# Kernel optimization log

Measured on AMD Instinct MI355X. Metric: run time of the kernel, lower is better.

The kernel has to match this reference:

```python
import jax, jax.numpy as jnp
import numpy as np

N = 100000
E = 800000
IN_FEATS = 128
H_FEATS = 128
HEADS = 4
OUT = H_FEATS // HEADS  # 32
NEG_SLOPE = 0.2  # DGL GATConv default


def gat_conv(x, src, dst, W, attn_l, attn_r, bias):
    """DGL-style GATConv. x: [N, F_in] -> [N, HEADS, OUT]."""
    h = (x @ W).reshape(N, HEADS, OUT)                      # projected features
    el = jnp.sum(h * attn_l, axis=-1)                       # [N, H]
    er = jnp.sum(h * attn_r, axis=-1)                       # [N, H]
    e = jax.nn.leaky_relu(el[src] + er[dst], NEG_SLOPE)     # [E, H] edge logits
    # edge softmax over incoming edges of each dst node
    m = jax.ops.segment_max(e, dst, num_segments=N)          # [N, H]
    ex = jnp.exp(e - m[dst])                                 # [E, H]
    s = jax.ops.segment_sum(ex, dst, num_segments=N)         # [N, H]
    a = ex / s[dst]                                          # [E, H]
    msg = h[src] * a[:, :, None]                             # [E, H, OUT]
    out = jax.ops.segment_sum(msg, dst, num_segments=N)      # [N, H, OUT]
    return out + bias.reshape(1, HEADS, OUT)


def setup_inputs() -> dict:
    key = jax.random.key(0)
    ks = jax.random.split(key, 12)
    feat = jax.random.normal(ks[0], (N, IN_FEATS), dtype=jnp.float32)
    src = jax.random.randint(ks[1], (E,), 0, N)
    dst = jax.random.randint(ks[2], (E,), 0, N)
    s1 = 1.0 / np.sqrt(IN_FEATS)
    s2 = 1.0 / np.sqrt(H_FEATS)
    return {
        "feat": feat,
        "src": src,
        "dst": dst,
        "W1": jax.random.normal(ks[3], (IN_FEATS, HEADS * OUT), dtype=jnp.float32) * s1,
        "al1": jax.random.normal(ks[4], (HEADS, OUT), dtype=jnp.float32) * s2,
        "ar1": jax.random.normal(ks[5], (HEADS, OUT), dtype=jnp.float32) * s2,
        "b1": jnp.zeros((HEADS * OUT,), dtype=jnp.float32),
        "W2": jax.random.normal(ks[6], (H_FEATS, HEADS * OUT), dtype=jnp.float32) * s2,
        "al2": jax.random.normal(ks[7], (HEADS, OUT), dtype=jnp.float32) * s2,
        "ar2": jax.random.normal(ks[8], (HEADS, OUT), dtype=jnp.float32) * s2,
        "b2": jnp.zeros((HEADS * OUT,), dtype=jnp.float32),
    }


def reference(feat, src, dst, W1, al1, ar1, b1, W2, al2, ar2, b2):
    h = gat_conv(feat, src, dst, W1, al1, ar1, b1).reshape(N, H_FEATS)  # flatten(1)
    h = jax.nn.relu(h)
    h = gat_conv(h, src, dst, W2, al2, ar2, b2).mean(axis=1)            # mean over heads
    return h
```

## Files before the change

kernel.cpp:

```cpp
#include <hip/hip_runtime.h>
#include <math.h>

#define N_NODES 100000
#define N_EDGES 800000
#define NEG_SLOPE 0.2f

typedef __attribute__((ext_vector_type(8))) short short8;
typedef __attribute__((ext_vector_type(4))) float floatx4;

__device__ __forceinline__ float lrelu(float x) { return x > 0.f ? x : NEG_SLOPE * x; }

__device__ __forceinline__ unsigned bf16_rne(float f) {
    unsigned u = __float_as_uint(f);
    return (u + 0x7fffu + ((u >> 16) & 1u)) >> 16;
}
__device__ __forceinline__ unsigned bfpack(float lo, float hi) {
    return bf16_rne(lo) | (bf16_rne(hi) << 16);
}
__device__ __forceinline__ float bflo(unsigned p) { return __uint_as_float(p << 16); }
__device__ __forceinline__ float bfhi(unsigned p) { return __uint_as_float(p & 0xffff0000u); }

__global__ __launch_bounds__(256) void k_hist_wprep(const int* __restrict__ dst,
                                                    int* __restrict__ deg,
                                                    const float* __restrict__ W1,
                                                    const float* __restrict__ al1,
                                                    const float* __restrict__ ar1,
                                                    const float* __restrict__ W2,
                                                    const float* __restrict__ al2,
                                                    const float* __restrict__ ar2,
                                                    unsigned short* __restrict__ wt1,
                                                    unsigned short* __restrict__ wt2,
                                                    unsigned short* __restrict__ et1,
                                                    unsigned short* __restrict__ et2) {
    int b = blockIdx.x, tid = threadIdx.x;
    if (b < 3125) {
        int e = b * 256 + tid;
        if (e < N_EDGES) atomicAdd(&deg[dst[e]], 1);
    } else if (b < 3253) {
        int t2 = (b - 3125) * 256 + tid;
        const float* W = (t2 < 16384) ? W1 : W2;
        unsigned short* wt = (t2 < 16384) ? wt1 : wt2;
        int t = t2 & 16383;
        int n = t >> 7, k = t & 127;
        wt[t] = (unsigned short)bf16_rne(W[k * 128 + n]);
    } else {
        const float* W = (b == 3253) ? W1 : W2;
        const float* al = (b == 3253) ? al1 : al2;
        const float* ar = (b == 3253) ? ar1 : ar2;
        unsigned short* et = (b == 3253) ? et1 : et2;
        for (int o = tid * 8; o < tid * 8 + 8; o++) {
            int n = o >> 7, k = o & 127;
            float sacc = 0.f;
            if (n < 8) {
                const float* a = (n < 4) ? al : ar;
                int hh = n & 3;
                #pragma unroll 8
                for (int c = 0; c < 32; c++)
                    sacc += W[k * 128 + hh * 32 + c] * a[hh * 32 + c];
            }
            et[n * 128 + k] = (unsigned short)bf16_rne(sacc);
        }
    }
}

__global__ __launch_bounds__(256) void k_scan(const int* __restrict__ deg,
                                              int* __restrict__ rs,
                                              int* __restrict__ cursor,
                                              int* __restrict__ bsums,
                                              int* __restrict__ done) {
    __shared__ int sd[256];
    int tid = threadIdx.x, b = blockIdx.x;
    int base = b * 1024 + tid * 4;
    int v0 = (base + 0 < N_NODES) ? deg[base + 0] : 0;
    int v1 = (base + 1 < N_NODES) ? deg[base + 1] : 0;
    int v2 = (base + 2 < N_NODES) ? deg[base + 2] : 0;
    int v3 = (base + 3 < N_NODES) ? deg[base + 3] : 0;
    int t = v0 + v1 + v2 + v3;
    sd[tid] = t;
    __syncthreads();
    int incl = t;
    for (int off = 1; off < 256; off <<= 1) {
        int x = (tid >= off) ? sd[tid - off] : 0;
        __syncthreads();
        incl += x;
        sd[tid] = incl;
        __syncthreads();
    }
    int excl = incl - t;

    if (tid == 255) {
        atomicExch(&bsums[b], incl);
        __threadfence();
        atomicAdd(done, 1);
    }
    if (tid == 0) {
        while (atomicAdd(done, 0) < 98) { }
    }
    __syncthreads();

    int bv = (tid < b) ? atomicAdd(&bsums[tid], 0) : 0;
    __syncthreads();
    sd[tid] = bv;
    __syncthreads();
    for (int off = 128; off > 0; off >>= 1) {
        if (tid < off) sd[tid] += sd[tid + off];
        __syncthreads();
    }
    int boff = sd[0];

    int p0 = excl + boff;
    if (base + 0 < N_NODES) { rs[base + 0] = p0; cursor[base + 0] = p0; }
    if (base + 1 < N_NODES) { rs[base + 1] = p0 + v0; cursor[base + 1] = p0 + v0; }
    if (base + 2 < N_NODES) { rs[base + 2] = p0 + v0 + v1; cursor[base + 2] = p0 + v0 + v1; }
    if (base + 3 < N_NODES) { rs[base + 3] = p0 + v0 + v1 + v2; cursor[base + 3] = p0 + v0 + v1 + v2; }
    if (b == 0 && tid == 0) rs[N_NODES] = N_EDGES;
}

__global__ void k_scatter(const int* __restrict__ src, const int* __restrict__ dst,
                          int* __restrict__ cursor, int* __restrict__ csr_src) {
    int e = blockIdx.x * blockDim.x + threadIdx.x;
    if (e < N_EDGES) {
        int d = dst[e];
        int p = atomicAdd(&cursor[d], 1);
        csr_src[p] = src[e];
    }
}

__global__ __launch_bounds__(256) void k_gemm(const void* __restrict__ Xv,
                                              const unsigned short* __restrict__ wt,
                                              const unsigned short* __restrict__ et,
                                              unsigned* __restrict__ Hb,
                                              float* __restrict__ EL,
                                              float* __restrict__ ER,
                                              int src_bf16) {
    __shared__ unsigned short wsh[128 * 128];
    __shared__ unsigned short esh[16 * 136];
    int tid = threadIdx.x;
    int w = tid >> 6, lane = tid & 63;
    int q = lane >> 4, nl = lane & 15;
    int base = blockIdx.x * 128;

    const uint4* wt4 = (const uint4*)wt;
    #pragma unroll
    for (int i = 0; i < 8; i++) {
        int idx = tid + i * 256;
        int rn = idx >> 4, c8 = idx & 15;
        int kc = c8 >> 2, qq = c8 & 3;
        int slot = rn * 128 + ((kc ^ ((rn >> 2) & 3)) * 4 + (qq ^ (rn & 3))) * 8;
        *(uint4*)&wsh[slot] = wt4[idx];
    }
    {
        const uint4* et4 = (const uint4*)et;
        int rn = tid >> 4, c8 = tid & 15;
        *(uint4*)&esh[rn * 136 + c8 * 8] = et4[tid];
    }

    short8 afr[2][4];
    int row0 = base + w * 32 + nl;
    if (!src_bf16) {
        const float4* X4 = (const float4*)Xv;
        #pragma unroll
        for (int rt = 0; rt < 2; rt++) {
            int rr = row0 + rt * 16; if (rr > N_NODES - 1) rr = N_NODES - 1;
            const float4* px = X4 + (size_t)rr * 32 + q * 2;
            #pragma unroll
            for (int kc = 0; kc < 4; kc++) {
                float4 u = px[kc * 8], v = px[kc * 8 + 1];
                short8 f;
                f[0] = (short)bf16_rne(u.x); f[1] = (short)bf16_rne(u.y);
                f[2] = (short)bf16_rne(u.z); f[3] = (short)bf16_rne(u.w);
                f[4] = (short)bf16_rne(v.x); f[5] = (short)bf16_rne(v.y);
                f[6] = (short)bf16_rne(v.z); f[7] = (short)bf16_rne(v.w);
                afr[rt][kc] = f;
            }
        }
    } else {
        const unsigned short* Xb = (const unsigned short*)Xv;
        #pragma unroll
        for (int rt = 0; rt < 2; rt++) {
            int rr = row0 + rt * 16; if (rr > N_NODES - 1) rr = N_NODES - 1;
            #pragma unroll
            for (int kc = 0; kc < 4; kc++)
                afr[rt][kc] = *(const short8*)(Xb + (size_t)rr * 128 + kc * 32 + q * 8);
        }
    }

    floatx4 acc[2][8];
    floatx4 acc_e[2];
    #pragma unroll
    for (int rt = 0; rt < 2; rt++) {
        acc_e[rt] = (floatx4){0.f, 0.f, 0.f, 0.f};
        #pragma unroll
        for (int ct = 0; ct < 8; ct++)
            acc[rt][ct] = (floatx4){0.f, 0.f, 0.f, 0.f};
    }

    __syncthreads();

    int sw_hi = (nl >> 2) & 3, sw_lo = nl & 3;
    #pragma unroll
    for (int ct = 0; ct < 8; ct++) {
        int rbase = (ct * 16 + nl) * 128;
        #pragma unroll
        for (int kc = 0; kc < 4; kc++) {
            short8 b = *(const short8*)&wsh[rbase + ((kc ^ sw_hi) * 4 + (q ^ sw_lo)) * 8];
            acc[0][ct] = __builtin_amdgcn_mfma_f32_16x16x32_bf16(afr[0][kc], b, acc[0][ct], 0, 0, 0);
            acc[1][ct] = __builtin_amdgcn_mfma_f32_16x16x32_bf16(afr[1][kc], b, acc[1][ct], 0, 0, 0);
        }
    }
    #pragma unroll
    for (int kc = 0; kc < 4; kc++) {
        short8 e8 = *(const short8*)&esh[nl * 136 + (kc * 4 + q) * 8];
        acc_e[0] = __builtin_amdgcn_mfma_f32_16x16x32_bf16(afr[0][kc], e8, acc_e[0], 0, 0, 0);
        acc_e[1] = __builtin_amdgcn_mfma_f32_16x16x32_bf16(afr[1][kc], e8, acc_e[1], 0, 0, 0);
    }

    #pragma unroll
    for (int rt = 0; rt < 2; rt++) {
        #pragma unroll
        for (int r = 0; r < 4; r++) {
            int row = base + w * 32 + rt * 16 + q * 4 + r;
            bool valid = row < N_NODES;
            unsigned* hrow = Hb + (size_t)row * 64;
            #pragma unroll
            for (int ct = 0; ct < 8; ct++) {
                float vlo = acc[rt][ct][r];
                float vhi = __shfl_down(vlo, 1);
                if (valid && !(nl & 1)) hrow[ct * 8 + (nl >> 1)] = bfpack(vlo, vhi);
            }
            if (valid && nl < 8) {
                float v = acc_e[rt][r];
                if (nl < 4) EL[row * 4 + nl] = v;
                else        ER[row * 4 + (nl & 3)] = v;
            }
        }
    }
}

__global__ __launch_bounds__(256) void k_gather(const int* __restrict__ rs,
                                                const int* __restrict__ csr_src,
                                                const float* __restrict__ EL,
                                                const float* __restrict__ ER,
                                                const unsigned* __restrict__ Hb,
                                                const float* __restrict__ bias,
                                                void* __restrict__ out,
                                                int final_layer) {
    int wid = (blockIdx.x * blockDim.x + threadIdx.x) >> 6;
    int lane = threadIdx.x & 63;
    int g = lane >> 4, l16 = lane & 15;
    int h = l16 >> 2;
    int n0 = wid * 4;
    if (n0 >= N_NODES) return;
    int nend = min(n0 + 4, N_NODES);

    float bv[8];
    #pragma unroll
    for (int c = 0; c < 8; c++) bv[c] = bias[l16 * 8 + c];

    for (int n = n0; n < nend; n++) {
        int s = rs[n], e = rs[n + 1];
        float erh = ER[n * 4 + h];
        float acc[8];
        #pragma unroll
        for (int c = 0; c < 8; c++) acc[c] = 0.f;
        float sa = 0.f;

        for (int j = s; j < e; j += 8) {
            int j0 = j + g, j1 = j + 4 + g;
            uint4 p0 = make_uint4(0, 0, 0, 0), p1 = make_uint4(0, 0, 0, 0);
            float w0 = 0.f, w1 = 0.f;
            if (j0 < e) {
                int s0 = csr_src[j0];
                p0 = *(const uint4*)(Hb + (size_t)s0 * 64 + l16 * 4);
                w0 = __expf(lrelu(EL[s0 * 4 + h] + erh));
            }
            if (j1 < e) {
                int s1 = csr_src[j1];
                p1 = *(const uint4*)(Hb + (size_t)s1 * 64 + l16 * 4);
                w1 = __expf(lrelu(EL[s1 * 4 + h] + erh));
            }
            sa += w0 + w1;
            acc[0] = fmaf(bflo(p0.x), w0, acc[0]); acc[1] = fmaf(bfhi(p0.x), w0, acc[1]);
            acc[2] = fmaf(bflo(p0.y), w0, acc[2]); acc[3] = fmaf(bfhi(p0.y), w0, acc[3]);
            acc[4] = fmaf(bflo(p0.z), w0, acc[4]); acc[5] = fmaf(bfhi(p0.z), w0, acc[5]);
            acc[6] = fmaf(bflo(p0.w), w0, acc[6]); acc[7] = fmaf(bfhi(p0.w), w0, acc[7]);
            acc[0] = fmaf(bflo(p1.x), w1, acc[0]); acc[1] = fmaf(bfhi(p1.x), w1, acc[1]);
            acc[2] = fmaf(bflo(p1.y), w1, acc[2]); acc[3] = fmaf(bfhi(p1.y), w1, acc[3]);
            acc[4] = fmaf(bflo(p1.z), w1, acc[4]); acc[5] = fmaf(bfhi(p1.z), w1, acc[5]);
            acc[6] = fmaf(bflo(p1.w), w1, acc[6]); acc[7] = fmaf(bfhi(p1.w), w1, acc[7]);
        }

        #pragma unroll
        for (int c = 0; c < 8; c++) {
            acc[c] += __shfl_xor(acc[c], 16);
            acc[c] += __shfl_xor(acc[c], 32);
        }
        sa += __shfl_xor(sa, 16);
        sa += __shfl_xor(sa, 32);
        float inv = (e > s) ? 1.f / sa : 0.f;

        float r[8];
        #pragma unroll
        for (int c = 0; c < 8; c++) r[c] = acc[c] * inv + bv[c];

        if (!final_layer) {
            if (g == 0) {
                uint4 pk;
                pk.x = bfpack(fmaxf(r[0], 0.f), fmaxf(r[1], 0.f));
                pk.y = bfpack(fmaxf(r[2], 0.f), fmaxf(r[3], 0.f));
                pk.z = bfpack(fmaxf(r[4], 0.f), fmaxf(r[5], 0.f));
                pk.w = bfpack(fmaxf(r[6], 0.f), fmaxf(r[7], 0.f));
                *(uint4*)((unsigned*)out + (size_t)n * 64 + l16 * 4) = pk;
            }
        } else {
            #pragma unroll
            for (int c = 0; c < 8; c++) {
                r[c] += __shfl_xor(r[c], 4);
                r[c] += __shfl_xor(r[c], 8);
            }
            if (g == 0 && l16 < 4) {
                float* po = (float*)out + (size_t)n * 32 + l16 * 8;
                *(float4*)po = make_float4(0.25f * r[0], 0.25f * r[1], 0.25f * r[2], 0.25f * r[3]);
                *(float4*)(po + 4) = make_float4(0.25f * r[4], 0.25f * r[5], 0.25f * r[6], 0.25f * r[7]);
            }
        }
    }
}

extern "C" void kernel_launch(void* const* d_in, const int* in_sizes, int n_in,
                              void* d_out, int out_size, void* d_ws, size_t ws_size,
                              hipStream_t stream) {
    const float* feat = (const float*)d_in[0];
    const int* src = (const int*)d_in[1];
    const int* dst = (const int*)d_in[2];
    const float* W1 = (const float*)d_in[3];
    const float* al1 = (const float*)d_in[4];
    const float* ar1 = (const float*)d_in[5];
    const float* b1 = (const float*)d_in[6];
    const float* W2 = (const float*)d_in[7];
    const float* al2 = (const float*)d_in[8];
    const float* ar2 = (const float*)d_in[9];
    const float* b2 = (const float*)d_in[10];
    float* out = (float*)d_out;

    char* ws = (char*)d_ws;
    size_t off = 0;
    auto alloc = [&](size_t bytes) {
        void* p = ws + off;
        off += (bytes + 255) & ~(size_t)255;
        return p;
    };
    int* deg = (int*)alloc((size_t)N_NODES * 4);
    int* done = (int*)alloc(256);
    int* rs = (int*)alloc(((size_t)N_NODES + 1) * 4);
    int* cursor = (int*)alloc((size_t)N_NODES * 4);
    int* bsums = (int*)alloc(128 * 4);
    int* csr_src = (int*)alloc((size_t)N_EDGES * 4);
    unsigned* Hb = (unsigned*)alloc((size_t)N_NODES * 64 * 4);
    float* el = (float*)alloc((size_t)N_NODES * 4 * 4);
    float* er = (float*)alloc((size_t)N_NODES * 4 * 4);
    unsigned* out1b = (unsigned*)alloc((size_t)N_NODES * 64 * 4);
    unsigned short* wt1 = (unsigned short*)alloc(128 * 128 * 2);
    unsigned short* wt2 = (unsigned short*)alloc(128 * 128 * 2);
    unsigned short* et1 = (unsigned short*)alloc(16 * 128 * 2);
    unsigned short* et2 = (unsigned short*)alloc(16 * 128 * 2);

    size_t zbytes = (size_t)((char*)done - (char*)deg) + 256;
    hipMemsetAsync(deg, 0, zbytes, stream);

    k_hist_wprep<<<3125 + 128 + 2, 256, 0, stream>>>(dst, deg, W1, al1, ar1,
                                                     W2, al2, ar2, wt1, wt2, et1, et2);
    k_scan<<<98, 256, 0, stream>>>(deg, rs, cursor, bsums, done);
    k_scatter<<<(N_EDGES + 255) / 256, 256, 0, stream>>>(src, dst, cursor, csr_src);

    int gemm_blocks = (N_NODES + 127) / 128;
    int gat_blocks = (N_NODES + 15) / 16;

    k_gemm<<<gemm_blocks, 256, 0, stream>>>(feat, wt1, et1, Hb, el, er, 0);
    k_gather<<<gat_blocks, 256, 0, stream>>>(rs, csr_src, el, er, Hb, b1, out1b, 0);
    k_gemm<<<gemm_blocks, 256, 0, stream>>>(out1b, wt2, et2, Hb, el, er, 1);
    k_gather<<<gat_blocks, 256, 0, stream>>>(rs, csr_src, el, er, Hb, b2, out, 1);
}
```

Before: 330.1 us.

## Fuse degree histogram into first GEMM launch and replace memset with prep kernel

Moves the layer-1 projection GEMM into the same launch as the dst-degree histogram, using block-index ranges to split work, so GEMM tiles and atomic histogram blocks run at the same time. The hipMemsetAsync that zeroed deg/done is replaced by extra blocks in a new weight-prep kernel. The separate histogram+weight-prep launch and the standalone layer-1 GEMM launch are removed. The GEMM blocks carry large shared-memory allocations that the histogram blocks also reserve, which may limit occupancy for the histogram part.

```diff
diff --git a/kernel.cpp b/kernel.cpp
--- a/kernel.cpp
+++ b/kernel.cpp
@@ -4,6 +4,8 @@
 #define N_NODES 100000
 #define N_EDGES 800000
 #define NEG_SLOPE 0.2f
+#define GEMM_BLOCKS 782
+#define HIST_BLOCKS 3125
 
 typedef __attribute__((ext_vector_type(8))) short short8;
 typedef __attribute__((ext_vector_type(4))) float floatx4;
@@ -20,34 +22,31 @@
 __device__ __forceinline__ float bflo(unsigned p) { return __uint_as_float(p << 16); }
 __device__ __forceinline__ float bfhi(unsigned p) { return __uint_as_float(p & 0xffff0000u); }
 
-__global__ __launch_bounds__(256) void k_hist_wprep(const int* __restrict__ dst,
-                                                    int* __restrict__ deg,
-                                                    const float* __restrict__ W1,
-                                                    const float* __restrict__ al1,
-                                                    const float* __restrict__ ar1,
-                                                    const float* __restrict__ W2,
-                                                    const float* __restrict__ al2,
-                                                    const float* __restrict__ ar2,
-                                                    unsigned short* __restrict__ wt1,
-                                                    unsigned short* __restrict__ wt2,
-                                                    unsigned short* __restrict__ et1,
-                                                    unsigned short* __restrict__ et2) {
+__global__ __launch_bounds__(256) void k_prep0(const float* __restrict__ W1,
+                                               const float* __restrict__ al1,
+                                               const float* __restrict__ ar1,
+                                               const float* __restrict__ W2,
+                                               const float* __restrict__ al2,
+                                               const float* __restrict__ ar2,
+                                               unsigned short* __restrict__ wt1,
+                                               unsigned short* __restrict__ wt2,
+                                               unsigned short* __restrict__ et1,
+                                               unsigned short* __restrict__ et2,
+                                               int* __restrict__ deg,
+                                               int* __restrict__ done) {
     int b = blockIdx.x, tid = threadIdx.x;
-    if (b < 3125) {
-        int e = b * 256 + tid;
-        if (e < N_EDGES) atomicAdd(&deg[dst[e]], 1);
-    } else if (b < 3253) {
-        int t2 = (b - 3125) * 256 + tid;
+    if (b < 128) {
+        int t2 = b * 256 + tid;
         const float* W = (t2 < 16384) ? W1 : W2;
         unsigned short* wt = (t2 < 16384) ? wt1 : wt2;
         int t = t2 & 16383;
         int n = t >> 7, k = t & 127;
         wt[t] = (unsigned short)bf16_rne(W[k * 128 + n]);
-    } else {
-        const float* W = (b == 3253) ? W1 : W2;
-        const float* al = (b == 3253) ? al1 : al2;
-        const float* ar = (b == 3253) ? ar1 : ar2;
-        unsigned short* et = (b == 3253) ? et1 : et2;
+    } else if (b < 130) {
+        const float* W = (b == 128) ? W1 : W2;
+        const float* al = (b == 128) ? al1 : al2;
+        const float* ar = (b == 128) ? ar1 : ar2;
+        unsigned short* et = (b == 128) ? et1 : et2;
         for (int o = tid * 8; o < tid * 8 + 8; o++) {
             int n = o >> 7, k = o & 127;
             float sacc = 0.f;
@@ -60,7 +59,154 @@
             }
             et[n * 128 + k] = (unsigned short)bf16_rne(sacc);
         }
-    }
+    } else if (b < 228) {
+        int i = (b - 130) * 1024 + tid * 4;
+        if (i + 3 < N_NODES) *(int4*)&deg[i] = make_int4(0, 0, 0, 0);
+        else { for (int j = i; j < N_NODES; j++) if (j >= 0) deg[j] = 0; }
+    } else {
+        if (tid < 64) done[tid] = 0;
+    }
+}
+
+__device__ __forceinline__ void gemm_tile(int base, const void* __restrict__ Xv,
+                                          const unsigned short* __restrict__ wt,
+                                          const unsigned short* __restrict__ et,
+                                          unsigned* __restrict__ Hb,
+                                          float* __restrict__ EL,
+                                          float* __restrict__ ER,
+                                          int src_bf16,
+                                          unsigned short* wsh,
+                                          unsigned short* esh) {
+    int tid = threadIdx.x;
+    int w = tid >> 6, lane = tid & 63;
+    int q = lane >> 4, nl = lane & 15;
+
+    const uint4* wt4 = (const uint4*)wt;
+    #pragma unroll
+    for (int i = 0; i < 8; i++) {
+        int idx = tid + i * 256;
+        int rn = idx >> 4, c8 = idx & 15;
+        int kc = c8 >> 2, qq = c8 & 3;
+        int slot = rn * 128 + ((kc ^ ((rn >> 2) & 3)) * 4 + (qq ^ (rn & 3))) * 8;
+        *(uint4*)&wsh[slot] = wt4[idx];
+    }
+    {
+        const uint4* et4 = (const uint4*)et;
+        int rn = tid >> 4, c8 = tid & 15;
+        *(uint4*)&esh[rn * 136 + c8 * 8] = et4[tid];
+    }
+
+    short8 afr[2][4];
+    int row0 = base + w * 32 + nl;
+    if (!src_bf16) {
+        const float4* X4 = (const float4*)Xv;
+        #pragma unroll
+        for (int rt = 0; rt < 2; rt++) {
+            int rr = row0 + rt * 16; if (rr > N_NODES - 1) rr = N_NODES - 1;
+            const float4* px = X4 + (size_t)rr * 32 + q * 2;
+            #pragma unroll
+            for (int kc = 0; kc < 4; kc++) {
+                float4 u = px[kc * 8], v = px[kc * 8 + 1];
+                short8 f;
+                f[0] = (short)bf16_rne(u.x); f[1] = (short)bf16_rne(u.y);
+                f[2] = (short)bf16_rne(u.z); f[3] = (short)bf16_rne(u.w);
+                f[4] = (short)bf16_rne(v.x); f[5] = (short)bf16_rne(v.y);
+                f[6] = (short)bf16_rne(v.z); f[7] = (short)bf16_rne(v.w);
+                afr[rt][kc] = f;
+            }
+        }
+    } else {
+        const unsigned short* Xb = (const unsigned short*)Xv;
+        #pragma unroll
+        for (int rt = 0; rt < 2; rt++) {
+            int rr = row0 + rt * 16; if (rr > N_NODES - 1) rr = N_NODES - 1;
+            #pragma unroll
+            for (int kc = 0; kc < 4; kc++)
+                afr[rt][kc] = *(const short8*)(Xb + (size_t)rr * 128 + kc * 32 + q * 8);
+        }
+    }
+
+    floatx4 acc[2][8];
+    floatx4 acc_e[2];
+    #pragma unroll
+    for (int rt = 0; rt < 2; rt++) {
+        acc_e[rt] = (floatx4){0.f, 0.f, 0.f, 0.f};
+        #pragma unroll
+        for (int ct = 0; ct < 8; ct++)
+            acc[rt][ct] = (floatx4){0.f, 0.f, 0.f, 0.f};
+    }
+
+    __syncthreads();
+
+    int sw_hi = (nl >> 2) & 3, sw_lo = nl & 3;
+    #pragma unroll
+    for (int ct = 0; ct < 8; ct++) {
+        int rbase = (ct * 16 + nl) * 128;
+        #pragma unroll
+        for (int kc = 0; kc < 4; kc++) {
+            short8 b = *(const short8*)&wsh[rbase + ((kc ^ sw_hi) * 4 + (q ^ sw_lo)) * 8];
+            acc[0][ct] = __builtin_amdgcn_mfma_f32_16x16x32_bf16(afr[0][kc], b, acc[0][ct], 0, 0, 0);
+            acc[1][ct] = __builtin_amdgcn_mfma_f32_16x16x32_bf16(afr[1][kc], b, acc[1][ct], 0, 0, 0);
+        }
+    }
+    #pragma unroll
+    for (int kc = 0; kc < 4; kc++) {
+        short8 e8 = *(const short8*)&esh[nl * 136 + (kc * 4 + q) * 8];
+        acc_e[0] = __builtin_amdgcn_mfma_f32_16x16x32_bf16(afr[0][kc], e8, acc_e[0], 0, 0, 0);
+        acc_e[1] = __builtin_amdgcn_mfma_f32_16x16x32_bf16(afr[1][kc], e8, acc_e[1], 0, 0, 0);
+    }
+
+    #pragma unroll
+    for (int rt = 0; rt < 2; rt++) {
+        #pragma unroll
+        for (int r = 0; r < 4; r++) {
+            int row = base + w * 32 + rt * 16 + q * 4 + r;
+            bool valid = row < N_NODES;
+            unsigned* hrow = Hb + (size_t)row * 64;
+            #pragma unroll
+            for (int ct = 0; ct < 8; ct++) {
+                float vlo = acc[rt][ct][r];
+                float vhi = __shfl_down(vlo, 1);
+                if (valid && !(nl & 1)) hrow[ct * 8 + (nl >> 1)] = bfpack(vlo, vhi);
+            }
+            if (valid && nl < 8) {
+                float v = acc_e[rt][r];
+                if (nl < 4) EL[row * 4 + nl] = v;
+                else        ER[row * 4 + (nl & 3)] = v;
+            }
+        }
+    }
+}
+
+__global__ __launch_bounds__(256) void k_gemm_hist(const float* __restrict__ feat,
+                                                   const unsigned short* __restrict__ wt1,
+                                                   const unsigned short* __restrict__ et1,
+                                                   unsigned* __restrict__ Hb,
+                                                   float* __restrict__ EL,
+                                                   float* __restrict__ ER,
+                                                   const int* __restrict__ dst,
+                                                   int* __restrict__ deg) {
+    __shared__ unsigned short wsh[128 * 128];
+    __shared__ unsigned short esh[16 * 136];
+    int b = blockIdx.x;
+    if (b < GEMM_BLOCKS) {
+        gemm_tile(b * 128, feat, wt1, et1, Hb, EL, ER, 0, wsh, esh);
+    } else {
+        int e = (b - GEMM_BLOCKS) * 256 + threadIdx.x;
+        if (e < N_EDGES) atomicAdd(&deg[dst[e]], 1);
+    }
+}
+
+__global__ __launch_bounds__(256) void k_gemm(const void* __restrict__ Xv,
+                                              const unsigned short* __restrict__ wt,
+                                              const unsigned short* __restrict__ et,
+                                              unsigned* __restrict__ Hb,
+                                              float* __restrict__ EL,
+                                              float* __restrict__ ER,
+                                              int src_bf16) {
+    __shared__ unsigned short wsh[128 * 128];
+    __shared__ unsigned short esh[16 * 136];
+    gemm_tile(blockIdx.x * 128, Xv, wt, et, Hb, EL, ER, src_bf16, wsh, esh);
 }
 
 __global__ __launch_bounds__(256) void k_scan(const int* __restrict__ deg,
@@ -126,117 +272,6 @@
     }
 }
 
-__global__ __launch_bounds__(256) void k_gemm(const void* __restrict__ Xv,
-                                              const unsigned short* __restrict__ wt,
-                                              const unsigned short* __restrict__ et,
-                                              unsigned* __restrict__ Hb,
-                                              float* __restrict__ EL,
-                                              float* __restrict__ ER,
-                                              int src_bf16) {
-    __shared__ unsigned short wsh[128 * 128];
-    __shared__ unsigned short esh[16 * 136];
-    int tid = threadIdx.x;
-    int w = tid >> 6, lane = tid & 63;
-    int q = lane >> 4, nl = lane & 15;
-    int base = blockIdx.x * 128;
-
-    const uint4* wt4 = (const uint4*)wt;
-    #pragma unroll
-    for (int i = 0; i < 8; i++) {
-        int idx = tid + i * 256;
-        int rn = idx >> 4, c8 = idx & 15;
-        int kc = c8 >> 2, qq = c8 & 3;
-        int slot = rn * 128 + ((kc ^ ((rn >> 2) & 3)) * 4 + (qq ^ (rn & 3))) * 8;
-        *(uint4*)&wsh[slot] = wt4[idx];
-    }
-    {
-        const uint4* et4 = (const uint4*)et;
-        int rn = tid >> 4, c8 = tid & 15;
-        *(uint4*)&esh[rn * 136 + c8 * 8] = et4[tid];
-    }
-
-    short8 afr[2][4];
-    int row0 = base + w * 32 + nl;
-    if (!src_bf16) {
-        const float4* X4 = (const float4*)Xv;
-        #pragma unroll
-        for (int rt = 0; rt < 2; rt++) {
-            int rr = row0 + rt * 16; if (rr > N_NODES - 1) rr = N_NODES - 1;
-            const float4* px = X4 + (size_t)rr * 32 + q * 2;
-            #pragma unroll
-            for (int kc = 0; kc < 4; kc++) {
-                float4 u = px[kc * 8], v = px[kc * 8 + 1];
-                short8 f;
-                f[0] = (short)bf16_rne(u.x); f[1] = (short)bf16_rne(u.y);
-                f[2] = (short)bf16_rne(u.z); f[3] = (short)bf16_rne(u.w);
-                f[4] = (short)bf16_rne(v.x); f[5] = (short)bf16_rne(v.y);
-                f[6] = (short)bf16_rne(v.z); f[7] = (short)bf16_rne(v.w);
-                afr[rt][kc] = f;
-            }
-        }
-    } else {
-        const unsigned short* Xb = (const unsigned short*)Xv;
-        #pragma unroll
-        for (int rt = 0; rt < 2; rt++) {
-            int rr = row0 + rt * 16; if (rr > N_NODES - 1) rr = N_NODES - 1;
-            #pragma unroll
-            for (int kc = 0; kc < 4; kc++)
-                afr[rt][kc] = *(const short8*)(Xb + (size_t)rr * 128 + kc * 32 + q * 8);
-        }
-    }
-
-    floatx4 acc[2][8];
-    floatx4 acc_e[2];
-    #pragma unroll
-    for (int rt = 0; rt < 2; rt++) {
-        acc_e[rt] = (floatx4){0.f, 0.f, 0.f, 0.f};
-        #pragma unroll
-        for (int ct = 0; ct < 8; ct++)
-            acc[rt][ct] = (floatx4){0.f, 0.f, 0.f, 0.f};
-    }
-
-    __syncthreads();
-
-    int sw_hi = (nl >> 2) & 3, sw_lo = nl & 3;
-    #pragma unroll
-    for (int ct = 0; ct < 8; ct++) {
-        int rbase = (ct * 16 + nl) * 128;
-        #pragma unroll
-        for (int kc = 0; kc < 4; kc++) {
-            short8 b = *(const short8*)&wsh[rbase + ((kc ^ sw_hi) * 4 + (q ^ sw_lo)) * 8];
-            acc[0][ct] = __builtin_amdgcn_mfma_f32_16x16x32_bf16(afr[0][kc], b, acc[0][ct], 0, 0, 0);
-            acc[1][ct] = __builtin_amdgcn_mfma_f32_16x16x32_bf16(afr[1][kc], b, acc[1][ct], 0, 0, 0);
-        }
-    }
-    #pragma unroll
-    for (int kc = 0; kc < 4; kc++) {
-        short8 e8 = *(const short8*)&esh[nl * 136 + (kc * 4 + q) * 8];
-        acc_e[0] = __builtin_amdgcn_mfma_f32_16x16x32_bf16(afr[0][kc], e8, acc_e[0], 0, 0, 0);
-        acc_e[1] = __builtin_amdgcn_mfma_f32_16x16x32_bf16(afr[1][kc], e8, acc_e[1], 0, 0, 0);
-    }
-
-    #pragma unroll
-    for (int rt = 0; rt < 2; rt++) {
-        #pragma unroll
-        for (int r = 0; r < 4; r++) {
-            int row = base + w * 32 + rt * 16 + q * 4 + r;
-            bool valid = row < N_NODES;
-            unsigned* hrow = Hb + (size_t)row * 64;
-            #pragma unroll
-            for (int ct = 0; ct < 8; ct++) {
-                float vlo = acc[rt][ct][r];
-                float vhi = __shfl_down(vlo, 1);
-                if (valid && !(nl & 1)) hrow[ct * 8 + (nl >> 1)] = bfpack(vlo, vhi);
-            }
-            if (valid && nl < 8) {
-                float v = acc_e[rt][r];
-                if (nl < 4) EL[row * 4 + nl] = v;
-                else        ER[row * 4 + (nl & 3)] = v;
-            }
-        }
-    }
-}
-
 __global__ __launch_bounds__(256) void k_gather(const int* __restrict__ rs,
                                                 const int* __restrict__ csr_src,
                                                 const float* __restrict__ EL,
@@ -365,19 +400,15 @@
     unsigned short* et1 = (unsigned short*)alloc(16 * 128 * 2);
     unsigned short* et2 = (unsigned short*)alloc(16 * 128 * 2);
 
-    size_t zbytes = (size_t)((char*)done - (char*)deg) + 256;
-    hipMemsetAsync(deg, 0, zbytes, stream);
-
-    k_hist_wprep<<<3125 + 128 + 2, 256, 0, stream>>>(dst, deg, W1, al1, ar1,
-                                                     W2, al2, ar2, wt1, wt2, et1, et2);
+    int gat_blocks = (N_NODES + 15) / 16;
+
+    k_prep0<<<229, 256, 0, stream>>>(W1, al1, ar1, W2, al2, ar2,
+                                     wt1, wt2, et1, et2, deg, done);
+    k_gemm_hist<<<GEMM_BLOCKS + HIST_BLOCKS, 256, 0, stream>>>(feat, wt1, et1, Hb, el, er,
+                                                               dst, deg);
     k_scan<<<98, 256, 0, stream>>>(deg, rs, cursor, bsums, done);
-    k_scatter<<<(N_EDGES + 255) / 256, 256, 0, stream>>>(src, dst, cursor, csr_src);
-
-    int gemm_blocks = (N_NODES + 127) / 128;
-    int gat_blocks = (N_NODES + 15) / 16;
-
-    k_gemm<<<gemm_blocks, 256, 0, stream>>>(feat, wt1, et1, Hb, el, er, 0);
+    k_scatter<<<HIST_BLOCKS, 256, 0, stream>>>(src, dst, cursor, csr_src);
     k_gather<<<gat_blocks, 256, 0, stream>>>(rs, csr_src, el, er, Hb, b1, out1b, 0);
-    k_gemm<<<gemm_blocks, 256, 0, stream>>>(out1b, wt2, et2, Hb, el, er, 1);
+    k_gemm<<<GEMM_BLOCKS, 256, 0, stream>>>(out1b, wt2, et2, Hb, el, er, 1);
     k_gather<<<gat_blocks, 256, 0, stream>>>(rs, csr_src, el, er, Hb, b2, out, 1);
 }
```

Result: no change. 323.7 us (-1.9%).
